# Optimization experiments

Measured on AMD Instinct MI355X. Metric: run time of the kernel, lower is better.

The kernel has to match this reference:

```python
import jax, jax.numpy as jnp
import numpy as np

N_NODES = 50000
N_EDGES = 800000


def spmm(edge_src, edge_dst, edge_weight, h):
    # out[i] = sum over edges (src->dst=i) of w * h[src]  == adj @ h
    msgs = h[edge_src] * edge_weight[:, None]  # [E, D]
    return jax.ops.segment_sum(msgs, edge_dst, num_segments=N_NODES)


def setup_inputs() -> dict:
    key = jax.random.key(0)
    ks = jax.random.split(key, 12)
    x = jax.random.normal(ks[0], (N_NODES, 512), dtype=jnp.float32)
    edge_src = jax.random.randint(ks[1], (N_EDGES,), 0, N_NODES, dtype=jnp.int32)
    edge_dst = jax.random.randint(ks[2], (N_EDGES,), 0, N_NODES, dtype=jnp.int32)
    edge_weight = jax.random.uniform(ks[3], (N_EDGES,), dtype=jnp.float32)
    def init_w(k, fin, fout):
        s = 1.0 / np.sqrt(fout)
        return jax.random.uniform(k, (fin, fout), minval=-s, maxval=s, dtype=jnp.float32)
    W1 = init_w(ks[4], 512, 512); b1 = jnp.zeros((512,), jnp.float32)
    W2 = init_w(ks[5], 512, 256); b2 = jnp.zeros((256,), jnp.float32)
    W3 = init_w(ks[6], 256, 128); b3 = jnp.zeros((128,), jnp.float32)
    W4 = init_w(ks[7], 128, 64);  b4 = jnp.zeros((64,), jnp.float32)
    return {"x": x, "edge_src": edge_src, "edge_dst": edge_dst,
            "edge_weight": edge_weight, "W1": W1, "b1": b1, "W2": W2,
            "b2": b2, "W3": W3, "b3": b3, "W4": W4, "b4": b4}


def reference(x, edge_src, edge_dst, edge_weight, W1, b1, W2, b2, W3, b3, W4, b4):
    # GraphConvolution: out = adj @ (x @ W) + b ; dropout is identity in eval mode
    def gc(h, W, b):
        return spmm(edge_src, edge_dst, edge_weight, h @ W) + b
    h = jax.nn.relu(gc(x, W1, b1))
    h = jax.nn.relu(gc(h, W2, b2))
    h = jax.nn.relu(gc(h, W3, b3))
    emb = gc(h, W4, b4)
    return emb
```

## Files before the change

### kernel.cpp

```cpp
#include <hip/hip_runtime.h>

#define NN 50000
#define NE 800000
#define SCAN_BLOCKS 196
#define CPAD 16
#define FILL_BLOCKS 3125

typedef __attribute__((ext_vector_type(8))) short short8;
typedef __attribute__((ext_vector_type(4))) float float4v;

struct __align__(8) us4 { unsigned short x, y, z, w; };
struct __align__(16) us8 { unsigned short v[8]; };

__device__ __forceinline__ unsigned short f2bf(float f) {
    unsigned u = __float_as_uint(f);
    unsigned r = (u + 0x7FFF + ((u >> 16) & 1)) >> 16;
    return (unsigned short)r;
}

__device__ __forceinline__ float bf2f(unsigned short u) {
    return __uint_as_float((unsigned)u << 16);
}

__device__ __forceinline__ void gload_lds16(const unsigned short* g, unsigned short* l) {
    __builtin_amdgcn_global_load_lds(
        (const __attribute__((address_space(1))) unsigned int*)g,
        (__attribute__((address_space(3))) unsigned int*)l,
        16, 0, 0);
}

template <int BM, int BN, int WM, int WN, int OUTBF, int FILL>
__global__ __launch_bounds__(256) void gemm_mfma(const unsigned short* __restrict__ A,
                                                 const unsigned short* __restrict__ Bt,
                                                 void* __restrict__ Cv,
                                                 int N, int K, int M, int gx,
                                                 const int* __restrict__ esrc,
                                                 const int* __restrict__ edst,
                                                 const float* __restrict__ ew,
                                                 int* __restrict__ cursor,
                                                 int2* __restrict__ csr) {
    constexpr int BK = 32;
    constexpr int MT = WM / 16;
    constexpr int NT = WN / 16;
    constexpr int WCOLS = BN / WN;

    __shared__ __align__(16) unsigned short As[2][BM * BK];
    __shared__ __align__(16) unsigned short Bs[2][BN * BK];

    int bx, by;
    if constexpr (FILL) {
        const int b = blockIdx.x;
        const int ngemm = gx * (M / BN);
        if (b >= ngemm) {
            int i = (b - ngemm) * 256 + threadIdx.x;
            for (; i < NE; i += FILL_BLOCKS * 256) {
                const int p = atomicAdd(&cursor[(size_t)edst[i] * CPAD], 1);
                csr[p] = make_int2(esrc[i], __float_as_int(ew[i]));
            }
            return;
        }
        bx = b % gx;
        by = b / gx;
    } else {
        bx = blockIdx.x;
        by = blockIdx.y;
    }

    const int tid = threadIdx.x;
    const int lane = tid & 63;
    const int wid = tid >> 6;
    const int col16 = lane & 15;
    const int q = lane >> 4;
    const int wr = (wid / WCOLS) * WM;
    const int wc = (wid % WCOLS) * WN;
    const int rowBase = bx * BM;
    const int colBase = by * BN;

    const int srow = lane >> 2;
    const int scol = ((lane & 3) ^ ((lane >> 3) & 3)) * 8;

    float4v acc[MT][NT];
#pragma unroll
    for (int t = 0; t < MT; ++t)
#pragma unroll
        for (int u = 0; u < NT; ++u)
            acc[t][u] = (float4v)0.f;

    auto stage = [&](int buf, int k0) {
#pragma unroll
        for (int l = wid; l < BM / 16; l += 4) {
            int row = rowBase + 16 * l + srow;
            row = row < N ? row : N - 1;
            gload_lds16(A + (size_t)row * K + k0 + scol, &As[buf][l * 512]);
        }
#pragma unroll
        for (int l = wid; l < BN / 16; l += 4) {
            const int row = colBase + 16 * l + srow;
            gload_lds16(Bt + (size_t)row * K + k0 + scol, &Bs[buf][l * 512]);
        }
    };

    const int frag = col16 * 32 + ((q ^ ((col16 >> 1) & 3))) * 8;
    const int awb = (wr / 16) * 512 + frag;
    const int bwb = (wc / 16) * 512 + frag;

    auto compute = [&](int buf) {
        short8 a[MT], b[NT];
#pragma unroll
        for (int t = 0; t < MT; ++t)
            a[t] = *(const short8*)&As[buf][awb + t * 512];
#pragma unroll
        for (int u = 0; u < NT; ++u)
            b[u] = *(const short8*)&Bs[buf][bwb + u * 512];
#pragma unroll
        for (int t = 0; t < MT; ++t)
#pragma unroll
            for (int u = 0; u < NT; ++u)
                acc[t][u] = __builtin_amdgcn_mfma_f32_16x16x32_bf16(a[t], b[u], acc[t][u], 0, 0, 0);
    };

    stage(0, 0);
    __syncthreads();
    int cur = 0;
    for (int k0 = BK; k0 < K; k0 += BK) {
        stage(cur ^ 1, k0);
        compute(cur);
        __syncthreads();
        cur ^= 1;
    }
    compute(cur);

#pragma unroll
    for (int t = 0; t < MT; ++t) {
        const int row0 = rowBase + wr + t * 16 + q * 4;
#pragma unroll
        for (int u = 0; u < NT; ++u) {
            const int col = colBase + wc + u * 16 + col16;
#pragma unroll
            for (int r = 0; r < 4; ++r) {
                const int row = row0 + r;
                if (row < N) {
                    if (OUTBF)
                        ((unsigned short*)Cv)[(size_t)row * M + col] = f2bf(acc[t][u][r]);
                    else
                        ((float*)Cv)[(size_t)row * M + col] = acc[t][u][r];
                }
            }
        }
    }
}

#define CH_BLOCKS 16000
__global__ void cvt_hist(const float* __restrict__ in, unsigned short* __restrict__ out,
                         const int* __restrict__ dst, int* __restrict__ counts) {
    const int b = blockIdx.x;
    if ((b % 5) != 4) {
        const int cb = (b / 5) * 4 + (b % 5);
        const long long n4 = (long long)NN * 512 / 4;
        long long i = (long long)cb * 256 + threadIdx.x;
        const long long stride = 12800LL * 256;
        for (; i < n4; i += stride) {
            const float4 v = *(const float4*)&in[i * 4];
            us4 o = {f2bf(v.x), f2bf(v.y), f2bf(v.z), f2bf(v.w)};
            *(us4*)&out[i * 4] = o;
        }
    } else {
        const int hb = b / 5;
        int i = hb * 256 + threadIdx.x;
        const int stride = 3200 * 256;
        for (; i < NE; i += stride) atomicAdd(&counts[(size_t)dst[i] * CPAD], 1);
    }
}

__global__ void cvt_transpose_all(const float* __restrict__ W1, unsigned short* __restrict__ Wt1,
                                  const float* __restrict__ W2, unsigned short* __restrict__ Wt2,
                                  const float* __restrict__ W3, unsigned short* __restrict__ Wt3,
                                  const float* __restrict__ W4, unsigned short* __restrict__ Wt4) {
    int idx = blockIdx.x * blockDim.x + threadIdx.x;
    const float* W; unsigned short* Wt; int K, M;
    if (idx < 262144)      { W = W1; Wt = Wt1; K = 512; M = 512; }
    else if (idx < 393216) { idx -= 262144; W = W2; Wt = Wt2; K = 512; M = 256; }
    else if (idx < 425984) { idx -= 393216; W = W3; Wt = Wt3; K = 256; M = 128; }
    else if (idx < 434176) { idx -= 425984; W = W4; Wt = Wt4; K = 128; M = 64; }
    else return;
    const int k = idx / M;
    const int m = idx % M;
    Wt[(size_t)m * K + k] = f2bf(W[(size_t)k * M + m]);
}

__global__ void zero_counts_pad(int4* __restrict__ counts4) {
    int i = blockIdx.x * blockDim.x + threadIdx.x;
    if (i < NN * CPAD / 4) counts4[i] = make_int4(0, 0, 0, 0);
}

__global__ __launch_bounds__(256) void scan_partial(const int* __restrict__ counts,
                                                    int* __restrict__ partials) {
    __shared__ int r[256];
    const int t = threadIdx.x;
    const int i = blockIdx.x * 256 + t;
    r[t] = (i < NN) ? counts[(size_t)i * CPAD] : 0;
    __syncthreads();
    for (int s = 128; s > 0; s >>= 1) {
        if (t < s) r[t] += r[t + s];
        __syncthreads();
    }
    if (t == 0) partials[blockIdx.x] = r[0];
}

__global__ __launch_bounds__(256) void scan_base(const int* __restrict__ partials,
                                                 int* __restrict__ bases,
                                                 int* __restrict__ offs) {
    __shared__ int s[256];
    const int t = threadIdx.x;
    const int v = (t < SCAN_BLOCKS) ? partials[t] : 0;
    s[t] = v;
    __syncthreads();
    for (int off = 1; off < 256; off <<= 1) {
        int x = (t >= off) ? s[t - off] : 0;
        __syncthreads();
        s[t] += x;
        __syncthreads();
    }
    if (t < SCAN_BLOCKS) bases[t] = s[t] - v;
    if (t == 255) offs[NN] = s[255];
}

__global__ __launch_bounds__(256) void scan_final(int* __restrict__ counts,
                                                  const int* __restrict__ bases,
                                                  int* __restrict__ offs) {
    __shared__ int s[256];
    const int t = threadIdx.x;
    const int i = blockIdx.x * 256 + t;
    const int v = (i < NN) ? counts[(size_t)i * CPAD] : 0;
    s[t] = v;
    __syncthreads();
    for (int off = 1; off < 256; off <<= 1) {
        int x = (t >= off) ? s[t - off] : 0;
        __syncthreads();
        s[t] += x;
        __syncthreads();
    }
    if (i < NN) {
        const int e = bases[blockIdx.x] + s[t] - v;
        offs[i] = e;
        counts[(size_t)i * CPAD] = e;
    }
}

template <int D, int RELU, int OUTBF>
__global__ __launch_bounds__(256) void spmm_gather(const int* __restrict__ offs,
                                                   const int2* __restrict__ csr,
                                                   const unsigned short* __restrict__ hp,
                                                   const float* __restrict__ bias,
                                                   void* __restrict__ outv,
                                                   int dbase, int dstride) {
    constexpr int TPN = D / 8;
    constexpr int NPB = 256 / TPN;
    const int tid = threadIdx.x;
    const int node = blockIdx.x * NPB + tid / TPN;
    const int d = dbase + (tid % TPN) * 8;
    if (node >= NN) return;
    const int beg = offs[node];
    const int end = offs[node + 1];

    float acc[8] = {};
    int j = beg;
    for (; j + 8 <= end; j += 8) {
        int2 e[8];
#pragma unroll
        for (int t = 0; t < 8; ++t) e[t] = csr[j + t];
        us8 h[8];
#pragma unroll
        for (int t = 0; t < 8; ++t)
            h[t] = *(const us8*)&hp[(long long)e[t].x * dstride + d];
#pragma unroll
        for (int t = 0; t < 8; ++t) {
            const float w = __int_as_float(e[t].y);
#pragma unroll
            for (int k = 0; k < 8; ++k) acc[k] += w * bf2f(h[t].v[k]);
        }
    }
    for (; j + 2 <= end; j += 2) {
        const int2 e0 = csr[j];
        const int2 e1 = csr[j + 1];
        const us8 h0 = *(const us8*)&hp[(long long)e0.x * dstride + d];
        const us8 h1 = *(const us8*)&hp[(long long)e1.x * dstride + d];
        const float w0 = __int_as_float(e0.y);
        const float w1 = __int_as_float(e1.y);
#pragma unroll
        for (int k = 0; k < 8; ++k)
            acc[k] += w0 * bf2f(h0.v[k]) + w1 * bf2f(h1.v[k]);
    }
    if (j < end) {
        const int2 e0 = csr[j];
        const us8 h0 = *(const us8*)&hp[(long long)e0.x * dstride + d];
        const float w0 = __int_as_float(e0.y);
#pragma unroll
        for (int k = 0; k < 8; ++k) acc[k] += w0 * bf2f(h0.v[k]);
    }
#pragma unroll
    for (int k = 0; k < 8; ++k) {
        acc[k] += bias[d + k];
        if (RELU) acc[k] = fmaxf(acc[k], 0.f);
    }
    if (OUTBF) {
        us8 o;
#pragma unroll
        for (int k = 0; k < 8; ++k) o.v[k] = f2bf(acc[k]);
        *(us8*)((unsigned short*)outv + (long long)node * dstride + d) = o;
    } else {
        float* op = (float*)outv + (long long)node * dstride + d;
        *(float4*)op = make_float4(acc[0], acc[1], acc[2], acc[3]);
        *(float4*)(op + 4) = make_float4(acc[4], acc[5], acc[6], acc[7]);
    }
}

extern "C" void kernel_launch(void* const* d_in, const int* in_sizes, int n_in,
                              void* d_out, int out_size, void* d_ws, size_t ws_size,
                              hipStream_t stream) {
    const float* x    = (const float*)d_in[0];
    const int*   esrc = (const int*)d_in[1];
    const int*   edst = (const int*)d_in[2];
    const float* ew   = (const float*)d_in[3];
    const float* W1 = (const float*)d_in[4];  const float* b1 = (const float*)d_in[5];
    const float* W2 = (const float*)d_in[6];  const float* b2 = (const float*)d_in[7];
    const float* W3 = (const float*)d_in[8];  const float* b3 = (const float*)d_in[9];
    const float* W4 = (const float*)d_in[10]; const float* b4 = (const float*)d_in[11];
    float* out = (float*)d_out;

    char* ws = (char*)d_ws;
    int*   offs    = (int*)ws;                    ws += (NN + 1) * sizeof(int);
    int*   partials= (int*)ws;                    ws += 256 * sizeof(int);
    int*   bases   = (int*)ws;                    ws += 256 * sizeof(int);
    ws = (char*)(((uintptr_t)ws + 63) & ~(uintptr_t)63);
    int*   counts  = (int*)ws;                    ws += (size_t)NN * CPAD * sizeof(int);
    int2*  csr     = (int2*)ws;                   ws += (size_t)NE * sizeof(int2);
    unsigned short* Wt1 = (unsigned short*)ws;    ws += 512 * 512 * sizeof(unsigned short);
    unsigned short* Wt2 = (unsigned short*)ws;    ws += 256 * 512 * sizeof(unsigned short);
    unsigned short* Wt3 = (unsigned short*)ws;    ws += 128 * 256 * sizeof(unsigned short);
    unsigned short* Wt4 = (unsigned short*)ws;    ws += 64 * 128 * sizeof(unsigned short);
    ws = (char*)(((uintptr_t)ws + 255) & ~(uintptr_t)255);
    unsigned short* tmp = (unsigned short*)ws;    ws += (size_t)NN * 512 * sizeof(unsigned short);
    ws = (char*)(((uintptr_t)ws + 255) & ~(uintptr_t)255);
    unsigned short* hb = (unsigned short*)ws;

    zero_counts_pad<<<(NN * CPAD / 4 + 255) / 256, 256, 0, stream>>>((int4*)counts);
    cvt_hist<<<CH_BLOCKS, 256, 0, stream>>>(x, hb, edst, counts);
    scan_partial<<<SCAN_BLOCKS, 256, 0, stream>>>(counts, partials);
    scan_base<<<1, 256, 0, stream>>>(partials, bases, offs);
    scan_final<<<SCAN_BLOCKS, 256, 0, stream>>>(counts, bases, offs);
    cvt_transpose_all<<<(434176 + 255) / 256, 256, 0, stream>>>(W1, Wt1, W2, Wt2, W3, Wt3, W4, Wt4);

    const int nby128 = (NN + 127) / 128;
    const int nby64  = (NN + 63) / 64;

    gemm_mfma<128, 128, 64, 64, 1, 1><<<nby128 * 4 + FILL_BLOCKS, 256, 0, stream>>>(
        hb, Wt1, tmp, NN, 512, 512, nby128, esrc, edst, ew, counts, csr);
    spmm_gather<512, 1, 1><<<NN / 4, 256, 0, stream>>>(offs, csr, tmp, b1, hb, 0, 512);
    gemm_mfma<128, 128, 64, 64, 1, 0><<<dim3(nby128, 2), 256, 0, stream>>>(
        hb, Wt2, tmp, NN, 512, 256, 0, nullptr, nullptr, nullptr, nullptr, nullptr);
    spmm_gather<256, 1, 1><<<NN / 8, 256, 0, stream>>>(offs, csr, tmp, b2, hb, 0, 256);
    gemm_mfma<64, 128, 32, 64, 1, 0><<<dim3(nby64, 1), 256, 0, stream>>>(
        hb, Wt3, tmp, NN, 256, 128, 0, nullptr, nullptr, nullptr, nullptr, nullptr);
    spmm_gather<128, 1, 1><<<NN / 16, 256, 0, stream>>>(offs, csr, tmp, b3, hb, 0, 128);
    gemm_mfma<64, 64, 32, 32, 1, 0><<<dim3(nby64, 1), 256, 0, stream>>>(
        hb, Wt4, tmp, NN, 128, 64, 0, nullptr, nullptr, nullptr, nullptr, nullptr);
    spmm_gather<64, 0, 0><<<(NN + 31) / 32, 256, 0, stream>>>(offs, csr, tmp, b4, out, 0, 64);
}
```

Baseline: 538.7 us.

## Partition SpMM feature columns across XCDs so each XCD's L2 holds one slice

Adds an SpMM gather kernel whose block index low bits select one of eight feature-column slices, so blocks scheduled round-robin onto the eight XCDs each touch only their own 1/8 of the gathered feature matrix. This aims to keep each XCD's L2 working set small enough to reuse gathered rows of h across nodes instead of re-fetching them from HBM. The cost is that each node's CSR edge list is read eight times and fewer threads work per node, with the partition relying on the hardware's round-robin block-to-XCD mapping. It is applied to the first three layers; the final 64-wide layer keeps the old kernel.

```diff
diff --git a/kernel.cpp b/kernel.cpp
--- a/kernel.cpp
+++ b/kernel.cpp
@@ -245,6 +245,69 @@
         offs[i] = e;
         counts[(size_t)i * CPAD] = e;
     }
+}
+
+template <int D, int RELU>
+__global__ __launch_bounds__(256) void spmm_gather_xcd(const int* __restrict__ offs,
+                                                       const int2* __restrict__ csr,
+                                                       const unsigned short* __restrict__ hp,
+                                                       const float* __restrict__ bias,
+                                                       unsigned short* __restrict__ outp) {
+    constexpr int PW = D / 8;
+    constexpr int TPNP = PW / 8;
+    constexpr int NPB = 256 / TPNP;
+    const int tid = threadIdx.x;
+    const int p = blockIdx.x & 7;
+    const int g = blockIdx.x >> 3;
+    const int node = g * NPB + tid / TPNP;
+    const int d = p * PW + (tid % TPNP) * 8;
+    if (node >= NN) return;
+    const int beg = offs[node];
+    const int end = offs[node + 1];
+
+    float acc[8] = {};
+    int j = beg;
+    for (; j + 8 <= end; j += 8) {
+        int2 e[8];
+#pragma unroll
+        for (int t = 0; t < 8; ++t) e[t] = csr[j + t];
+        us8 h[8];
+#pragma unroll
+        for (int t = 0; t < 8; ++t)
+            h[t] = *(const us8*)&hp[(long long)e[t].x * D + d];
+#pragma unroll
+        for (int t = 0; t < 8; ++t) {
+            const float w = __int_as_float(e[t].y);
+#pragma unroll
+            for (int k = 0; k < 8; ++k) acc[k] += w * bf2f(h[t].v[k]);
+        }
+    }
+    for (; j + 2 <= end; j += 2) {
+        const int2 e0 = csr[j];
+        const int2 e1 = csr[j + 1];
+        const us8 h0 = *(const us8*)&hp[(long long)e0.x * D + d];
+        const us8 h1 = *(const us8*)&hp[(long long)e1.x * D + d];
+        const float w0 = __int_as_float(e0.y);
+        const float w1 = __int_as_float(e1.y);
+#pragma unroll
+        for (int k = 0; k < 8; ++k)
+            acc[k] += w0 * bf2f(h0.v[k]) + w1 * bf2f(h1.v[k]);
+    }
+    if (j < end) {
+        const int2 e0 = csr[j];
+        const us8 h0 = *(const us8*)&hp[(long long)e0.x * D + d];
+        const float w0 = __int_as_float(e0.y);
+#pragma unroll
+        for (int k = 0; k < 8; ++k) acc[k] += w0 * bf2f(h0.v[k]);
+    }
+    us8 o;
+#pragma unroll
+    for (int k = 0; k < 8; ++k) {
+        float v = acc[k] + bias[d + k];
+        if (RELU) v = fmaxf(v, 0.f);
+        o.v[k] = f2bf(v);
+    }
+    *(us8*)&outp[(long long)node * D + d] = o;
 }
 
 template <int D, int RELU, int OUTBF>
@@ -356,13 +419,13 @@
 
     gemm_mfma<128, 128, 64, 64, 1, 1><<<nby128 * 4 + FILL_BLOCKS, 256, 0, stream>>>(
         hb, Wt1, tmp, NN, 512, 512, nby128, esrc, edst, ew, counts, csr);
-    spmm_gather<512, 1, 1><<<NN / 4, 256, 0, stream>>>(offs, csr, tmp, b1, hb, 0, 512);
+    spmm_gather_xcd<512, 1><<<8 * ((NN + 31) / 32), 256, 0, stream>>>(offs, csr, tmp, b1, hb);
     gemm_mfma<128, 128, 64, 64, 1, 0><<<dim3(nby128, 2), 256, 0, stream>>>(
         hb, Wt2, tmp, NN, 512, 256, 0, nullptr, nullptr, nullptr, nullptr, nullptr);
-    spmm_gather<256, 1, 1><<<NN / 8, 256, 0, stream>>>(offs, csr, tmp, b2, hb, 0, 256);
+    spmm_gather_xcd<256, 1><<<8 * ((NN + 63) / 64), 256, 0, stream>>>(offs, csr, tmp, b2, hb);
     gemm_mfma<64, 128, 32, 64, 1, 0><<<dim3(nby64, 1), 256, 0, stream>>>(
         hb, Wt3, tmp, NN, 256, 128, 0, nullptr, nullptr, nullptr, nullptr, nullptr);
-    spmm_gather<128, 1, 1><<<NN / 16, 256, 0, stream>>>(offs, csr, tmp, b3, hb, 0, 128);
+    spmm_gather_xcd<128, 1><<<8 * ((NN + 127) / 128), 256, 0, stream>>>(offs, csr, tmp, b3, hb);
     gemm_mfma<64, 64, 32, 32, 1, 0><<<dim3(nby64, 1), 256, 0, stream>>>(
         hb, Wt4, tmp, NN, 128, 64, 0, nullptr, nullptr, nullptr, nullptr, nullptr);
     spmm_gather<64, 0, 0><<<(NN + 31) / 32, 256, 0, stream>>>(offs, csr, tmp, b4, out, 0, 64);
```

New measurement: 600.9 us. 11.5% more time.
